# Kernel tuning notes

Measured on AMD Instinct MI355X. Metric: run time of the kernel, lower is better.

Reference implementation:

```python
import jax, jax.numpy as jnp
import numpy as np

H = 100  # hidden size


def _lstm_final_hidden(x, W_ih, W_hh, b_ih, b_hh):
    # x: [B, T, 4] -> final hidden state h_T: [B, H]
    B, T, _ = x.shape
    # Precompute input contribution for all time steps: [B, T, 4H]
    xW = jnp.einsum('btf,gf->btg', x, W_ih) + b_ih + b_hh
    xW = jnp.transpose(xW, (1, 0, 2))  # [T, B, 4H] for scan over time

    def step(carry, xt):
        h, c = carry
        gates = xt + h @ W_hh.T  # [B, 4H]
        i, f, g, o = jnp.split(gates, 4, axis=-1)  # torch gate order: i, f, g, o
        c = jax.nn.sigmoid(f) * c + jax.nn.sigmoid(i) * jnp.tanh(g)
        h = jax.nn.sigmoid(o) * jnp.tanh(c)
        return (h, c), None

    h0 = jnp.zeros((B, H), dtype=x.dtype)
    (hT, _), _ = jax.lax.scan(step, (h0, h0), xW)
    return hT


def setup_inputs() -> dict:
    key = jax.random.key(0)
    k1, k2, k3, k4, k5 = jax.random.split(key, 5)
    n_cells, T = 4096, 128
    short_ttf = jax.random.normal(k1, (n_cells, 3, T, 4), dtype=jnp.float32)
    W_ih = jax.random.normal(k2, (4 * H, 4), dtype=jnp.float32) * 0.1
    # torch init: uniform(-0.05, 0.05) for weight_hh
    W_hh = jax.random.uniform(k3, (4 * H, H), dtype=jnp.float32, minval=-0.05, maxval=0.05)
    b_ih = jax.random.normal(k4, (4 * H,), dtype=jnp.float32) * 0.1
    b_hh = jax.random.normal(k5, (4 * H,), dtype=jnp.float32) * 0.1
    return {"short_ttf": short_ttf, "W_ih": W_ih, "W_hh": W_hh, "b_ih": b_ih, "b_hh": b_hh}


def reference(short_ttf, W_ih, W_hh, b_ih, b_hh):
    # short_ttf: [n_cells, 3, T, 4]. Each of the 3 sub-sequences per cell is run
    # through the same LSTM; last-step hidden states are concatenated -> [n_cells, 3H].
    n_cells, three, T, F = short_ttf.shape
    x = short_ttf.reshape(n_cells * three, T, F)  # batch all sequences together
    hT = _lstm_final_hidden(x, W_ih, W_hh, b_ih, b_hh)  # [n_cells*3, H]
    return hT.reshape(n_cells, three * H)  # [n_cells, 300]
```

## Files before the change

### kernel.cpp

```cpp
#include <hip/hip_runtime.h>
#include <cstdint>


#define H_UNITS 100
#define T_STEPS 128
#define S_BLK   16
#define NSEQ    12288
#define NBLK    (NSEQ / S_BLK)
#define NTILE   25
#define KSTR    136
#define LOG2E   1.4426950408889634f
#define TWO_L   2.8853900817779268f

typedef __attribute__((ext_vector_type(8))) _Float16 halfx8;
typedef __attribute__((ext_vector_type(8))) unsigned short ushortx8;
typedef __attribute__((ext_vector_type(4))) float floatx4;

__device__ __forceinline__ unsigned short f32_to_f16u(float x) {
    _Float16 h = (_Float16)x;
    return __builtin_bit_cast(unsigned short, h);
}
__device__ __forceinline__ float f16u_to_f32(unsigned short u) {
    _Float16 h = __builtin_bit_cast(_Float16, u);
    return (float)h;
}
#if __has_builtin(__builtin_amdgcn_exp2f)
__device__ __forceinline__ float fexp2(float x) { return __builtin_amdgcn_exp2f(x); }
#else
__device__ __forceinline__ float fexp2(float x) { return exp2f(x); }
#endif

__global__ void lstm_prep_pack(const float* __restrict__ W_ih,
                               const float* __restrict__ W_hh,
                               const float* __restrict__ b_ih,
                               const float* __restrict__ b_hh,
                               ushortx8* __restrict__ Bpack) {
    int t = blockIdx.x * 256 + threadIdx.x;
    if (t >= NTILE * 4 * 64) return;
    int lane = t & 63;
    int kc   = (t >> 6) & 3;
    int tile = t >> 8;
    int m    = lane & 15;
    int n  = (m & 3) * 100 + tile * 4 + (m >> 2);
    float sc = (n >= 200 && n < 300) ? (2.0f * LOG2E) : LOG2E;
    int k0 = kc * 32 + ((lane >> 4) & 3) * 8;
    ushortx8 v;
#pragma unroll
    for (int j = 0; j < 8; ++j) {
        int k = k0 + j;
        unsigned short w = 0;
        if (k < 96) {
            int u = ((k >> 3) << 3) + ((k & 1) << 2) + ((k & 7) >> 1);
            w = f32_to_f16u(W_hh[n * 100 + u] * sc);
        } else if (k < 104) {
            if (!(k & 1)) {
                int u = 96 + ((k - 96) >> 1);
                w = f32_to_f16u(W_hh[n * 100 + u] * sc);
            }
        } else if (k < 112) {
            int c = (k - 104) >> 1;
            w = f32_to_f16u(W_ih[n * 4 + c] * sc);
        } else if (k < 120) {
            if (!(k & 1)) {
                int c = (k - 112) >> 1;
                float wf = W_ih[n * 4 + c] * sc;
                unsigned short hi = f32_to_f16u(wf);
                w = f32_to_f16u(wf - f16u_to_f32(hi));
            }
        } else if (k == 120) {
            float bb = (b_ih[n] + b_hh[n]) * sc;
            w = f32_to_f16u(bb);
        } else if (k == 122) {
            float bb = (b_ih[n] + b_hh[n]) * sc;
            unsigned short hi = f32_to_f16u(bb);
            w = f32_to_f16u(bb - f16u_to_f32(hi));
        }
        v[j] = w;
    }
    Bpack[t] = v;
}

__global__ void __launch_bounds__(256, 3)
lstm_main(const float* __restrict__ x, const ushortx8* __restrict__ Bpack,
          float* __restrict__ out) {
    __shared__ __align__(16) unsigned short s_A[2][16 * KSTR];
    __shared__ __align__(16) ushortx8       s_W[NTILE * 64];

    const int tid  = threadIdx.x;
    const int lane = tid & 63;
    const int wavu = __builtin_amdgcn_readfirstlane(tid >> 6);
    const int seq0 = blockIdx.x * S_BLK;
    const int m    = lane & 15;
    const int quad = lane >> 4;

    halfx8 wfrag[7][3];
#pragma unroll
    for (int it = 0; it < 7; ++it) {
        int tile = wavu + it * 4;
        if (tile < NTILE) {
#pragma unroll
            for (int kc = 0; kc < 3; ++kc)
                wfrag[it][kc] = __builtin_bit_cast(halfx8, Bpack[(tile * 4 + kc + 1) * 64 + lane]);
        }
    }
    for (int i = tid; i < NTILE * 64; i += 256)
        s_W[i] = Bpack[(i >> 6) * 256 + (i & 63)];

    const int rt = tid - 128;
    const int rs = rt & 15, rc = (rt >> 4) & 7;
    const float* xb = x + (size_t)(seq0 + rs) * (T_STEPS * 4) + (rc & 3);

    for (int i = tid; i < (2 * 16 * KSTR) / 2; i += 256)
        ((unsigned int*)s_A)[i] = 0u;
    float x0 = 0.0f;
    if (tid >= 128) x0 = xb[0];
    __syncthreads();
    if (tid >= 128) {
        unsigned short hi = f32_to_f16u(x0);
        if (rc < 4) {
            s_A[0][rs * KSTR + 104 + 2 * rc] = hi;
            s_A[0][rs * KSTR + 112 + 2 * rc] = hi;
        } else {
            s_A[0][rs * KSTR + 105 + 2 * (rc - 4)] =
                f32_to_f16u(x0 - f16u_to_f32(hi));
        }
    } else if (tid < 32) {
        s_A[tid >> 4][(tid & 15) * KSTR + 120] = 0x3C00;
    } else if (tid < 64) {
        int d = tid - 32;
        s_A[d >> 4][(d & 15) * KSTR + 122] = 0x3C00;
    }
    __syncthreads();

    float c_reg[6];
#pragma unroll
    for (int it = 0; it < 6; ++it) c_reg[it] = 0.0f;
    float c24 = 0.0f;

    const int rowOff = m * KSTR;
    const int aOff   = rowOff + quad * 8;
    const int q2     = quad << 1;
    int hbase[7];
#pragma unroll
    for (int it = 0; it < 7; ++it) {
        int tile = wavu + it * 4;
        hbase[it] = (tile < 24) ? (((tile >> 1) << 3) + (tile & 1)) : 96;
    }

    for (int t = 0; t < T_STEPS; ++t) {
        const int bR = t & 1;
        const unsigned short* base  = s_A[bR];
        unsigned short*       baseW = s_A[bR ^ 1];

        float xnext = 0.0f;
        if (tid >= 128) {
            int tn = t + 1; if (tn > T_STEPS - 1) tn = T_STEPS - 1;
            xnext = xb[tn * 4];
        }

        halfx8 hh[4];
#pragma unroll
        for (int kc = 0; kc < 4; ++kc)
            hh[kc] = *(const halfx8*)(base + aOff + kc * 32);

        const bool last = (t == T_STEPS - 1);

        auto docell = [&](int tile, int wbase, halfx8 w1, halfx8 w2, halfx8 w3, float& cm) {
            halfx8 w0 = __builtin_bit_cast(halfx8, s_W[tile * 64 + lane]);
            floatx4 acc = {0.0f, 0.0f, 0.0f, 0.0f};
            acc = __builtin_amdgcn_mfma_f32_16x16x32_f16(w0, hh[0], acc, 0, 0, 0);
            acc = __builtin_amdgcn_mfma_f32_16x16x32_f16(w1, hh[1], acc, 0, 0, 0);
            acc = __builtin_amdgcn_mfma_f32_16x16x32_f16(w2, hh[2], acc, 0, 0, 0);
            acc = __builtin_amdgcn_mfma_f32_16x16x32_f16(w3, hh[3], acc, 0, 0, 0);
            float ei = fexp2(acc[0]);
            float ef = fexp2(acc[1]);
            float eg = fexp2(acc[2]);
            float eo = fexp2(acc[3]);
            float a  = 1.0f + ei, b = 1.0f + ef;
            float d  = eg + 1.0f;
            float e2s = fmaf(eg, TWO_L, -TWO_L);
            float q  = a * d;
            float r  = __builtin_amdgcn_rcpf(q * b);
            float nm = fmaf(ef * q, cm, (ei * b) * e2s);
            float c2 = nm * r;
            cm = c2;
            float cc = fminf(c2, 115.0f);
            float ec = fexp2(cc);
            float r2 = __builtin_amdgcn_rcpf((1.0f + eo) * (ec + 1.0f));
            float h  = (eo * (ec - 1.0f)) * r2;
            if (!last) {
                baseW[rowOff + wbase + q2] = f32_to_f16u(h);
            } else {
                int j = tile * 4 + quad;
                out[(size_t)(seq0 + m) * H_UNITS + j] = h;
            }
        };

#pragma unroll
        for (int it = 0; it < 6; ++it)
            docell(wavu + it * 4, hbase[it], wfrag[it][0], wfrag[it][1], wfrag[it][2], c_reg[it]);
        if (wavu == 0)
            docell(24, hbase[6], wfrag[6][0], wfrag[6][1], wfrag[6][2], c24);

        if (tid >= 128 && !last) {
            unsigned short hi = f32_to_f16u(xnext);
            if (rc < 4) {
                baseW[rs * KSTR + 104 + 2 * rc] = hi;
                baseW[rs * KSTR + 112 + 2 * rc] = hi;
            } else {
                baseW[rs * KSTR + 105 + 2 * (rc - 4)] =
                    f32_to_f16u(xnext - f16u_to_f32(hi));
            }
        }
        __syncthreads();
    }
}

extern "C" void kernel_launch(void* const* d_in, const int* in_sizes, int n_in,
                              void* d_out, int out_size, void* d_ws, size_t ws_size,
                              hipStream_t stream) {
    const float* x    = (const float*)d_in[0];
    const float* W_ih = (const float*)d_in[1];
    const float* W_hh = (const float*)d_in[2];
    const float* b_ih = (const float*)d_in[3];
    const float* b_hh = (const float*)d_in[4];
    ushortx8* Bpack = (ushortx8*)d_ws;

    lstm_prep_pack<<<25, 256, 0, stream>>>(W_ih, W_hh, b_ih, b_hh, Bpack);
    lstm_main<<<NBLK, 256, 0, stream>>>(x, Bpack, (float*)d_out);
}
```

Baseline: 286.7 us.

## Process 48 sequences per block with register-resident weights reused across groups

Each block now has 8 waves and handles three 16-sequence groups instead of one. Every wave keeps all four K-chunks of its weight tiles in registers, so the LDS weight buffer is gone and each weight fragment is reused across the three groups. The goal is to amortise weight loads and per-step barriers over more sequences and to cut LDS traffic. In exchange each wave does more serial gate work per time step, and the launch gives fewer, larger blocks, which lowers wave-level parallelism per CU.

```diff
diff --git a/kernel.cpp b/kernel.cpp
--- a/kernel.cpp
+++ b/kernel.cpp
@@ -4,11 +4,12 @@
 
 #define H_UNITS 100
 #define T_STEPS 128
-#define S_BLK   16
+#define SEQ_BLK 48
 #define NSEQ    12288
-#define NBLK    (NSEQ / S_BLK)
-#define NTILE   25
+#define NBLK    (NSEQ / SEQ_BLK)
 #define KSTR    136
+#define GRP     (16 * KSTR)
+#define BUFU    (3 * GRP)
 #define LOG2E   1.4426950408889634f
 #define TWO_L   2.8853900817779268f
 
@@ -36,7 +37,7 @@
                                const float* __restrict__ b_hh,
                                ushortx8* __restrict__ Bpack) {
     int t = blockIdx.x * 256 + threadIdx.x;
-    if (t >= NTILE * 4 * 64) return;
+    if (t >= 25 * 4 * 64) return;
     int lane = t & 63;
     int kc   = (t >> 6) & 3;
     int tile = t >> 8;
@@ -80,37 +81,48 @@
     Bpack[t] = v;
 }
 
-__global__ void __launch_bounds__(256, 3)
+__global__ void __launch_bounds__(512, 2)
 lstm_main(const float* __restrict__ x, const ushortx8* __restrict__ Bpack,
           float* __restrict__ out) {
-    __shared__ __align__(16) unsigned short s_A[2][16 * KSTR];
-    __shared__ __align__(16) ushortx8       s_W[NTILE * 64];
+    __shared__ __align__(16) unsigned short s_A[2 * BUFU];
 
     const int tid  = threadIdx.x;
     const int lane = tid & 63;
     const int wavu = __builtin_amdgcn_readfirstlane(tid >> 6);
-    const int seq0 = blockIdx.x * S_BLK;
+    const int seq0 = blockIdx.x * SEQ_BLK;
     const int m    = lane & 15;
     const int quad = lane >> 4;
-
-    halfx8 wfrag[7][3];
-#pragma unroll
-    for (int it = 0; it < 7; ++it) {
-        int tile = wavu + it * 4;
-        if (tile < NTILE) {
-#pragma unroll
-            for (int kc = 0; kc < 3; ++kc)
-                wfrag[it][kc] = __builtin_bit_cast(halfx8, Bpack[(tile * 4 + kc + 1) * 64 + lane]);
-        }
-    }
-    for (int i = tid; i < NTILE * 64; i += 256)
-        s_W[i] = Bpack[(i >> 6) * 256 + (i & 63)];
-
-    const int rt = tid - 128;
-    const int rs = rt & 15, rc = (rt >> 4) & 7;
+    const int q2   = quad << 1;
+
+    halfx8 wfrag[4][4];
+#pragma unroll
+    for (int it = 0; it < 3; ++it) {
+        int tile = wavu + it * 8;
+#pragma unroll
+        for (int kc = 0; kc < 4; ++kc)
+            wfrag[it][kc] = __builtin_bit_cast(halfx8, Bpack[(tile * 4 + kc) * 64 + lane]);
+    }
+    if (wavu < 3) {
+#pragma unroll
+        for (int kc = 0; kc < 4; ++kc)
+            wfrag[3][kc] = __builtin_bit_cast(halfx8, Bpack[(24 * 4 + kc) * 64 + lane]);
+    }
+
+    int wb[3];
+#pragma unroll
+    for (int it = 0; it < 3; ++it) {
+        int tile = wavu + it * 8;
+        wb[it] = ((tile >> 1) << 3) + (tile & 1);
+    }
+
+    const int rt   = tid - 128;
+    const int rtc  = rt < 0 ? 0 : rt;
+    const int rs   = rtc >> 3;
+    const int rc   = rtc & 7;
+    const int roff = (rs >> 4) * GRP + (rs & 15) * KSTR;
     const float* xb = x + (size_t)(seq0 + rs) * (T_STEPS * 4) + (rc & 3);
 
-    for (int i = tid; i < (2 * 16 * KSTR) / 2; i += 256)
+    for (int i = tid; i < BUFU; i += 512)
         ((unsigned int*)s_A)[i] = 0u;
     float x0 = 0.0f;
     if (tid >= 128) x0 = xb[0];
@@ -118,39 +130,32 @@
     if (tid >= 128) {
         unsigned short hi = f32_to_f16u(x0);
         if (rc < 4) {
-            s_A[0][rs * KSTR + 104 + 2 * rc] = hi;
-            s_A[0][rs * KSTR + 112 + 2 * rc] = hi;
+            s_A[roff + 104 + 2 * rc] = hi;
+            s_A[roff + 112 + 2 * rc] = hi;
         } else {
-            s_A[0][rs * KSTR + 105 + 2 * (rc - 4)] =
+            s_A[roff + 105 + 2 * (rc - 4)] =
                 f32_to_f16u(x0 - f16u_to_f32(hi));
         }
-    } else if (tid < 32) {
-        s_A[tid >> 4][(tid & 15) * KSTR + 120] = 0x3C00;
-    } else if (tid < 64) {
-        int d = tid - 32;
-        s_A[d >> 4][(d & 15) * KSTR + 122] = 0x3C00;
+    } else if (tid < 96) {
+        int b = tid / 48, r = tid % 48, g = r / 16, s = r & 15;
+        s_A[b * BUFU + g * GRP + s * KSTR + 120] = 0x3C00;
+        s_A[b * BUFU + g * GRP + s * KSTR + 122] = 0x3C00;
     }
     __syncthreads();
 
-    float c_reg[6];
-#pragma unroll
-    for (int it = 0; it < 6; ++it) c_reg[it] = 0.0f;
+    float c9[3][3];
+#pragma unroll
+    for (int it = 0; it < 3; ++it)
+#pragma unroll
+        for (int g = 0; g < 3; ++g) c9[it][g] = 0.0f;
     float c24 = 0.0f;
 
-    const int rowOff = m * KSTR;
-    const int aOff   = rowOff + quad * 8;
-    const int q2     = quad << 1;
-    int hbase[7];
-#pragma unroll
-    for (int it = 0; it < 7; ++it) {
-        int tile = wavu + it * 4;
-        hbase[it] = (tile < 24) ? (((tile >> 1) << 3) + (tile & 1)) : 96;
-    }
+    const int aRow = m * KSTR + quad * 8;
 
     for (int t = 0; t < T_STEPS; ++t) {
         const int bR = t & 1;
-        const unsigned short* base  = s_A[bR];
-        unsigned short*       baseW = s_A[bR ^ 1];
+        const unsigned short* baseR = s_A + bR * BUFU;
+        unsigned short*       baseW = s_A + (bR ^ 1) * BUFU;
 
         float xnext = 0.0f;
         if (tid >= 128) {
@@ -158,20 +163,22 @@
             xnext = xb[tn * 4];
         }
 
-        halfx8 hh[4];
-#pragma unroll
-        for (int kc = 0; kc < 4; ++kc)
-            hh[kc] = *(const halfx8*)(base + aOff + kc * 32);
+        halfx8 hh[3][4];
+#pragma unroll
+        for (int g = 0; g < 3; ++g)
+#pragma unroll
+            for (int kc = 0; kc < 4; ++kc)
+                hh[g][kc] = *(const halfx8*)(baseR + g * GRP + aRow + kc * 32);
 
         const bool last = (t == T_STEPS - 1);
 
-        auto docell = [&](int tile, int wbase, halfx8 w1, halfx8 w2, halfx8 w3, float& cm) {
-            halfx8 w0 = __builtin_bit_cast(halfx8, s_W[tile * 64 + lane]);
+        auto docell = [&](const halfx8* w, const halfx8* hhg, float& cm,
+                          int wbase, int jb, int g) {
             floatx4 acc = {0.0f, 0.0f, 0.0f, 0.0f};
-            acc = __builtin_amdgcn_mfma_f32_16x16x32_f16(w0, hh[0], acc, 0, 0, 0);
-            acc = __builtin_amdgcn_mfma_f32_16x16x32_f16(w1, hh[1], acc, 0, 0, 0);
-            acc = __builtin_amdgcn_mfma_f32_16x16x32_f16(w2, hh[2], acc, 0, 0, 0);
-            acc = __builtin_amdgcn_mfma_f32_16x16x32_f16(w3, hh[3], acc, 0, 0, 0);
+            acc = __builtin_amdgcn_mfma_f32_16x16x32_f16(w[0], hhg[0], acc, 0, 0, 0);
+            acc = __builtin_amdgcn_mfma_f32_16x16x32_f16(w[1], hhg[1], acc, 0, 0, 0);
+            acc = __builtin_amdgcn_mfma_f32_16x16x32_f16(w[2], hhg[2], acc, 0, 0, 0);
+            acc = __builtin_amdgcn_mfma_f32_16x16x32_f16(w[3], hhg[3], acc, 0, 0, 0);
             float ei = fexp2(acc[0]);
             float ef = fexp2(acc[1]);
             float eg = fexp2(acc[2]);
@@ -189,26 +196,29 @@
             float r2 = __builtin_amdgcn_rcpf((1.0f + eo) * (ec + 1.0f));
             float h  = (eo * (ec - 1.0f)) * r2;
             if (!last) {
-                baseW[rowOff + wbase + q2] = f32_to_f16u(h);
+                baseW[g * GRP + m * KSTR + wbase + q2] = f32_to_f16u(h);
             } else {
-                int j = tile * 4 + quad;
-                out[(size_t)(seq0 + m) * H_UNITS + j] = h;
+                out[(size_t)(seq0 + g * 16 + m) * H_UNITS + jb + quad] = h;
             }
         };
 
 #pragma unroll
-        for (int it = 0; it < 6; ++it)
-            docell(wavu + it * 4, hbase[it], wfrag[it][0], wfrag[it][1], wfrag[it][2], c_reg[it]);
-        if (wavu == 0)
-            docell(24, hbase[6], wfrag[6][0], wfrag[6][1], wfrag[6][2], c24);
+        for (int it = 0; it < 3; ++it)
+#pragma unroll
+            for (int g = 0; g < 3; ++g)
+                docell(wfrag[it], hh[g], c9[it][g], wb[it], (wavu + it * 8) * 4, g);
+
+        if (wavu == 0)      docell(wfrag[3], hh[0], c24, 96, 96, 0);
+        else if (wavu == 1) docell(wfrag[3], hh[1], c24, 96, 96, 1);
+        else if (wavu == 2) docell(wfrag[3], hh[2], c24, 96, 96, 2);
 
         if (tid >= 128 && !last) {
             unsigned short hi = f32_to_f16u(xnext);
             if (rc < 4) {
-                baseW[rs * KSTR + 104 + 2 * rc] = hi;
-                baseW[rs * KSTR + 112 + 2 * rc] = hi;
+                baseW[roff + 104 + 2 * rc] = hi;
+                baseW[roff + 112 + 2 * rc] = hi;
             } else {
-                baseW[rs * KSTR + 105 + 2 * (rc - 4)] =
+                baseW[roff + 105 + 2 * (rc - 4)] =
                     f32_to_f16u(xnext - f16u_to_f32(hi));
             }
         }
@@ -227,5 +237,5 @@
     ushortx8* Bpack = (ushortx8*)d_ws;
 
     lstm_prep_pack<<<25, 256, 0, stream>>>(W_ih, W_hh, b_ih, b_hh, Bpack);
-    lstm_main<<<NBLK, 256, 0, stream>>>(x, Bpack, (float*)d_out);
-}
+    lstm_main<<<NBLK, 512, 0, stream>>>(x, Bpack, (float*)d_out);
+}
```

New measurement: 302.1 us. 5.4% more time.

## Keep all weight fragments in registers and batch MFMAs before activations

Applied to the files above, without the earlier changes.

All four K-chunks of the weight fragments now live in registers, so the shared-memory weight buffer and its per-step LDS reads go away. The launch bound drops from 3 to 2 blocks per SM to leave room for the extra registers. The step loop is split so that all MFMA chains for a wave are issued first and the activation math runs afterwards, which gives more independent matrix work to hide latency. The cost is fewer resident blocks, so less latency hiding between blocks, plus higher register pressure.

```diff
diff --git a/kernel.cpp b/kernel.cpp
--- a/kernel.cpp
+++ b/kernel.cpp
@@ -80,11 +80,10 @@
     Bpack[t] = v;
 }
 
-__global__ void __launch_bounds__(256, 3)
+__global__ void __launch_bounds__(256, 2)
 lstm_main(const float* __restrict__ x, const ushortx8* __restrict__ Bpack,
           float* __restrict__ out) {
     __shared__ __align__(16) unsigned short s_A[2][16 * KSTR];
-    __shared__ __align__(16) ushortx8       s_W[NTILE * 64];
 
     const int tid  = threadIdx.x;
     const int lane = tid & 63;
@@ -92,19 +91,25 @@
     const int seq0 = blockIdx.x * S_BLK;
     const int m    = lane & 15;
     const int quad = lane >> 4;
-
-    halfx8 wfrag[7][3];
+    const int q2   = quad << 1;
+
+    halfx8 wfrag[7][4];
 #pragma unroll
     for (int it = 0; it < 7; ++it) {
         int tile = wavu + it * 4;
         if (tile < NTILE) {
 #pragma unroll
-            for (int kc = 0; kc < 3; ++kc)
-                wfrag[it][kc] = __builtin_bit_cast(halfx8, Bpack[(tile * 4 + kc + 1) * 64 + lane]);
-        }
-    }
-    for (int i = tid; i < NTILE * 64; i += 256)
-        s_W[i] = Bpack[(i >> 6) * 256 + (i & 63)];
+            for (int kc = 0; kc < 4; ++kc)
+                wfrag[it][kc] = __builtin_bit_cast(halfx8, Bpack[(tile * 4 + kc) * 64 + lane]);
+        }
+    }
+
+    int wb[7];
+#pragma unroll
+    for (int it = 0; it < 7; ++it) {
+        int tile = wavu + it * 4;
+        wb[it] = (tile < 24) ? (((tile >> 1) << 3) + (tile & 1)) : 96;
+    }
 
     const int rt = tid - 128;
     const int rs = rt & 15, rc = (rt >> 4) & 7;
@@ -132,20 +137,12 @@
     }
     __syncthreads();
 
-    float c_reg[6];
-#pragma unroll
-    for (int it = 0; it < 6; ++it) c_reg[it] = 0.0f;
-    float c24 = 0.0f;
+    float c_reg[7];
+#pragma unroll
+    for (int it = 0; it < 7; ++it) c_reg[it] = 0.0f;
 
     const int rowOff = m * KSTR;
     const int aOff   = rowOff + quad * 8;
-    const int q2     = quad << 1;
-    int hbase[7];
-#pragma unroll
-    for (int it = 0; it < 7; ++it) {
-        int tile = wavu + it * 4;
-        hbase[it] = (tile < 24) ? (((tile >> 1) << 3) + (tile & 1)) : 96;
-    }
 
     for (int t = 0; t < T_STEPS; ++t) {
         const int bR = t & 1;
@@ -165,13 +162,15 @@
 
         const bool last = (t == T_STEPS - 1);
 
-        auto docell = [&](int tile, int wbase, halfx8 w1, halfx8 w2, halfx8 w3, float& cm) {
-            halfx8 w0 = __builtin_bit_cast(halfx8, s_W[tile * 64 + lane]);
-            floatx4 acc = {0.0f, 0.0f, 0.0f, 0.0f};
-            acc = __builtin_amdgcn_mfma_f32_16x16x32_f16(w0, hh[0], acc, 0, 0, 0);
-            acc = __builtin_amdgcn_mfma_f32_16x16x32_f16(w1, hh[1], acc, 0, 0, 0);
-            acc = __builtin_amdgcn_mfma_f32_16x16x32_f16(w2, hh[2], acc, 0, 0, 0);
-            acc = __builtin_amdgcn_mfma_f32_16x16x32_f16(w3, hh[3], acc, 0, 0, 0);
+        auto gemm4 = [&](const halfx8* w) {
+            floatx4 a = {0.0f, 0.0f, 0.0f, 0.0f};
+            a = __builtin_amdgcn_mfma_f32_16x16x32_f16(w[0], hh[0], a, 0, 0, 0);
+            a = __builtin_amdgcn_mfma_f32_16x16x32_f16(w[1], hh[1], a, 0, 0, 0);
+            a = __builtin_amdgcn_mfma_f32_16x16x32_f16(w[2], hh[2], a, 0, 0, 0);
+            a = __builtin_amdgcn_mfma_f32_16x16x32_f16(w[3], hh[3], a, 0, 0, 0);
+            return a;
+        };
+        auto activate = [&](floatx4 acc, float& cm, int wbase, int jb) {
             float ei = fexp2(acc[0]);
             float ef = fexp2(acc[1]);
             float eg = fexp2(acc[2]);
@@ -191,16 +190,21 @@
             if (!last) {
                 baseW[rowOff + wbase + q2] = f32_to_f16u(h);
             } else {
-                int j = tile * 4 + quad;
-                out[(size_t)(seq0 + m) * H_UNITS + j] = h;
+                out[(size_t)(seq0 + m) * H_UNITS + jb + quad] = h;
             }
         };
 
+        floatx4 acc[6];
 #pragma unroll
         for (int it = 0; it < 6; ++it)
-            docell(wavu + it * 4, hbase[it], wfrag[it][0], wfrag[it][1], wfrag[it][2], c_reg[it]);
-        if (wavu == 0)
-            docell(24, hbase[6], wfrag[6][0], wfrag[6][1], wfrag[6][2], c24);
+            acc[it] = gemm4(wfrag[it]);
+        floatx4 acc24;
+        if (wavu == 0) acc24 = gemm4(wfrag[6]);
+
+#pragma unroll
+        for (int it = 0; it < 6; ++it)
+            activate(acc[it], c_reg[it], wb[it], (wavu + it * 4) * 4);
+        if (wavu == 0) activate(acc24, c_reg[6], wb[6], 96);
 
         if (tid >= 128 && !last) {
             unsigned short hi = f32_to_f16u(xnext);
```

After: 295.6 us. 1.03x slower.
